# Performance work log

Measured on AMD Instinct MI355X. Metric: run time of the kernel, lower is better.

## Reference

```python
import jax, jax.numpy as jnp
import numpy as np

N_NODES = 100000
N_EDGES = 1600000
NFEAT = 128
NHID = 128
NCLASS = 16


def _sage_conv(x, src, dst, w_self, w_neigh, b):
    # mean aggregation over in-neighbors: for each dst, mean of x[src]
    msgs = x[src]                                   # [E, F] gather
    agg = jax.ops.segment_sum(msgs, dst, num_segments=x.shape[0])  # [N, F]
    deg = jax.ops.segment_sum(jnp.ones((src.shape[0],), x.dtype), dst,
                              num_segments=x.shape[0])             # [N]
    h_neigh = agg / jnp.maximum(deg, 1.0)[:, None]
    return x @ w_self + h_neigh @ w_neigh + b


def setup_inputs() -> dict:
    key = jax.random.key(0)
    ks = jax.random.split(key, 9)
    x = jax.random.normal(ks[0], (N_NODES, NFEAT), dtype=jnp.float32)
    src = jax.random.randint(ks[1], (N_EDGES,), 0, N_NODES, dtype=jnp.int32)
    dst = jax.random.randint(ks[2], (N_EDGES,), 0, N_NODES, dtype=jnp.int32)
    s1 = 1.0 / np.sqrt(NFEAT)
    s2 = 1.0 / np.sqrt(NHID)
    w_self1 = jax.random.uniform(ks[3], (NFEAT, NHID), jnp.float32, -s1, s1)
    w_neigh1 = jax.random.uniform(ks[4], (NFEAT, NHID), jnp.float32, -s1, s1)
    b1 = jnp.zeros((NHID,), jnp.float32)
    w_self2 = jax.random.uniform(ks[5], (NHID, NCLASS), jnp.float32, -s2, s2)
    w_neigh2 = jax.random.uniform(ks[6], (NHID, NCLASS), jnp.float32, -s2, s2)
    b2 = jnp.zeros((NCLASS,), jnp.float32)
    return {"x": x, "src": src, "dst": dst,
            "w_self1": w_self1, "w_neigh1": w_neigh1, "b1": b1,
            "w_self2": w_self2, "w_neigh2": w_neigh2, "b2": b2}


def reference(x, src, dst, w_self1, w_neigh1, b1, w_self2, w_neigh2, b2):
    h = jax.nn.relu(_sage_conv(x, src, dst, w_self1, w_neigh1, b1))
    # dropout is identity in eval mode (training=False)
    out = _sage_conv(h, src, dst, w_self2, w_neigh2, b2)
    return jax.nn.log_softmax(out, axis=1)
```

## Files before the change

kernel.cpp:

```cpp
#include <hip/hip_runtime.h>
#include <math.h>

#define NN 100000
#define NE 1600000
#define BSZ 64
#define NBUCK ((NN + BSZ - 1) / BSZ)
#define NBLK 256
#define CHUNK ((NE + NBLK - 1) / NBLK)
#define NH (NBUCK * NBLK)
#define NSB ((NH + 1023) / 1024)

typedef unsigned int uint;
typedef unsigned short ushort_t;
typedef float f32x2 __attribute__((ext_vector_type(2)));
typedef float f32x4 __attribute__((ext_vector_type(4)));
typedef short s16x8 __attribute__((ext_vector_type(8)));

union U4S8 { uint4 u; s16x8 s; };

__device__ inline uint bf16_1(float f) {
  uint u = __float_as_uint(f);
  return (u + 0x7FFFu + ((u >> 16) & 1u)) >> 16;
}
__device__ inline uint bf16_2(float lo, float hi) {
  return bf16_1(lo) | (bf16_1(hi) << 16);
}

__device__ inline f32x4 mfma_bf16(uint4 a, uint4 b, f32x4 c) {
  U4S8 ua, ub; ua.u = a; ub.u = b;
  return __builtin_amdgcn_mfma_f32_16x16x32_bf16(ua.s, ub.s, c, 0, 0, 0);
}

__global__ __launch_bounds__(256) void tobf16_kernel(
    const float* __restrict__ x, uint* __restrict__ xh,
    uint* __restrict__ xq) {
  int i = blockIdx.x * 256 + threadIdx.x;
  if (i >= NN * 16) return;
  const float4* p = (const float4*)x + (size_t)i * 2;
  float4 a = p[0], b = p[1];
  uint4 o;
  o.x = bf16_2(a.x, a.y);
  o.y = bf16_2(a.z, a.w);
  o.z = bf16_2(b.x, b.y);
  o.w = bf16_2(b.z, b.w);
  ((uint4*)xh)[i] = o;
  int q0 = __builtin_amdgcn_cvt_pk_fp8_f32(a.x, a.y, 0, false);
  q0 = __builtin_amdgcn_cvt_pk_fp8_f32(a.z, a.w, q0, true);
  int q1 = __builtin_amdgcn_cvt_pk_fp8_f32(b.x, b.y, 0, false);
  q1 = __builtin_amdgcn_cvt_pk_fp8_f32(b.z, b.w, q1, true);
  uint2 oq; oq.x = (uint)q0; oq.y = (uint)q1;
  int r = i >> 4;
  int u = (i & 15) * 2;
  *(uint2*)(xq + (size_t)r * 32 + u) = oq;
}

__global__ __launch_bounds__(256) void prep_w_kernel(
    const float* __restrict__ ws1, const float* __restrict__ wn1,
    const float* __restrict__ ws2, const float* __restrict__ wn2,
    uint* __restrict__ w1t, uint* __restrict__ w2t) {
  int idx = blockIdx.x * 256 + threadIdx.x;
  if (idx < 128 * 128) {
    int col = idx >> 7, ku = idx & 127;
    int k = ku * 2;
    const float* w = (k < 128) ? ws1 : wn1;
    int kk = (k < 128) ? k : (k - 128);
    w1t[idx] = bf16_2(w[(size_t)kk * 128 + col], w[(size_t)(kk + 1) * 128 + col]);
  } else if (idx < 128 * 128 + 32 * 64) {
    int j = idx - 128 * 128;
    int col = j >> 6, ku = j & 63;
    int k = ku * 2;
    const float* w = (col < 16) ? ws2 : wn2;
    int c = col & 15;
    w2t[j] = bf16_2(w[(size_t)k * 16 + c], w[(size_t)(k + 1) * 16 + c]);
  }
}

__global__ __launch_bounds__(1024) void histA_kernel(
    const int* __restrict__ dst, int* __restrict__ hist2) {
  __shared__ int lh[NBUCK];
  int tid = threadIdx.x;
  int b = blockIdx.x;
  for (int i = tid; i < NBUCK; i += 1024) lh[i] = 0;
  __syncthreads();
  int e0 = b * CHUNK, e1 = min(e0 + CHUNK, NE);
  for (int e = e0 + tid; e < e1; e += 1024) {
    atomicAdd(&lh[dst[e] >> 6], 1);
  }
  __syncthreads();
  for (int i = tid; i < NBUCK; i += 1024)
    hist2[(size_t)b * NBUCK + i] = lh[i];
}

__global__ __launch_bounds__(1024) void transpose_kernel(
    const int* __restrict__ hist2, int* __restrict__ hist) {
  __shared__ int t[32][33];
  int tx = threadIdx.x & 31, ty = threadIdx.x >> 5;
  int i = blockIdx.x * 32 + tx;
  int b = blockIdx.y * 32 + ty;
  if (i < NBUCK) t[ty][tx] = hist2[(size_t)b * NBUCK + i];
  __syncthreads();
  int i2 = blockIdx.x * 32 + ty;
  int b2 = blockIdx.y * 32 + tx;
  if (i2 < NBUCK) hist[(size_t)i2 * NBLK + b2] = t[tx][ty];
}

__global__ __launch_bounds__(1024) void scan_sums_kernel(
    const int* __restrict__ hist, int* __restrict__ sums) {
  __shared__ int sdata[1024];
  int i = blockIdx.x * 1024 + threadIdx.x;
  sdata[threadIdx.x] = (i < NH) ? hist[i] : 0;
  __syncthreads();
#pragma unroll
  for (int s = 512; s > 0; s >>= 1) {
    if (threadIdx.x < s) sdata[threadIdx.x] += sdata[threadIdx.x + s];
    __syncthreads();
  }
  if (threadIdx.x == 0) sums[blockIdx.x] = sdata[0];
}

__global__ __launch_bounds__(512) void scan_tops_kernel(int* __restrict__ sums) {
  __shared__ int buf[2][512];
  int tid = threadIdx.x;
  int v = (tid < NSB) ? sums[tid] : 0;
  buf[0][tid] = v;
  __syncthreads();
  int pp = 0;
#pragma unroll
  for (int d = 1; d < 512; d <<= 1) {
    buf[pp ^ 1][tid] = buf[pp][tid] + ((tid >= d) ? buf[pp][tid - d] : 0);
    pp ^= 1;
    __syncthreads();
  }
  if (tid < NSB) sums[tid] = buf[pp][tid] - v;
}

__global__ __launch_bounds__(1024) void scan_apply_kernel(
    int* __restrict__ hist, const int* __restrict__ sums) {
  __shared__ int buf[2][1024];
  int tid = threadIdx.x;
  int i = blockIdx.x * 1024 + tid;
  int v = (i < NH) ? hist[i] : 0;
  buf[0][tid] = v;
  __syncthreads();
  int pp = 0;
#pragma unroll
  for (int d = 1; d < 1024; d <<= 1) {
    buf[pp ^ 1][tid] = buf[pp][tid] + ((tid >= d) ? buf[pp][tid - d] : 0);
    pp ^= 1;
    __syncthreads();
  }
  if (i < NH) hist[i] = sums[blockIdx.x] + buf[pp][tid] - v;
}

__global__ __launch_bounds__(1024) void scatter3_kernel(
    const int* __restrict__ src, const int* __restrict__ dst,
    const int* __restrict__ scanned, unsigned int* __restrict__ ebuf) {
  __shared__ int cur[NBUCK];
  int tid = threadIdx.x;
  int b = blockIdx.x;
  for (int i = tid; i < NBUCK; i += 1024) cur[i] = scanned[i * NBLK + b];
  __syncthreads();
  int e0 = b * CHUNK, e1 = min(e0 + CHUNK, NE);
  for (int e = e0 + tid; e < e1; e += 1024) {
    int d = dst[e];
    int p = atomicAdd(&cur[d >> 6], 1);
    ebuf[p] = ((unsigned int)(d & 63) << 17) | (unsigned int)src[e];
  }
}

__global__ __launch_bounds__(256) void bucket_sort_kernel(
    const unsigned int* __restrict__ ebuf, const int* __restrict__ scanned,
    int* __restrict__ deg, int* __restrict__ off, int* __restrict__ perm) {
  __shared__ int cnt[BSZ];
  __shared__ int loc_off[BSZ];
  int tid = threadIdx.x;
  int b = blockIdx.x;
  int e0 = scanned[b * NBLK];
  int e1 = (b + 1 < NBUCK) ? scanned[(b + 1) * NBLK] : NE;

  if (tid < BSZ) cnt[tid] = 0;
  __syncthreads();
  for (int e = e0 + tid; e < e1; e += 256)
    atomicAdd(&cnt[ebuf[e] >> 17], 1);
  __syncthreads();

  if (tid < BSZ) {
    int v = cnt[tid];
    int incl = v;
#pragma unroll
    for (int d = 1; d < 64; d <<= 1) {
      int t = __shfl_up(incl, d);
      if (tid >= d) incl += t;
    }
    int excl = incl - v;
    loc_off[tid] = e0 + excl;
    int node = b * BSZ + tid;
    if (node < NN) { off[node] = e0 + excl; deg[node] = v; }
    cnt[tid] = 0;
  }
  __syncthreads();

  for (int e = e0 + tid; e < e1; e += 256) {
    unsigned int pk = ebuf[e];
    int dl = pk >> 17;
    int p = loc_off[dl] + atomicAdd(&cnt[dl], 1);
    perm[p] = (int)(pk & 0x1FFFF);
  }
}

__global__ __launch_bounds__(256) void mean1_kernel(
    const uint* __restrict__ xq, const int* __restrict__ off,
    const int* __restrict__ deg, const int* __restrict__ perm,
    uint* __restrict__ m1h) {
  int node = blockIdx.x * 4 + (threadIdx.x >> 6);
  int lane = threadIdx.x & 63;
  if (node >= NN) return;
  int o = off[node], dg = deg[node];
  int slot = lane >> 5;
  int q = lane & 31;
  f32x2 a0 = {0.f, 0.f}, a1 = {0.f, 0.f};
  int j = 0;
  for (; j + 8 <= dg; j += 8) {
    int sA = perm[o + j + slot];
    int sB = perm[o + j + 2 + slot];
    int sC = perm[o + j + 4 + slot];
    int sD = perm[o + j + 6 + slot];
    uint vA = xq[(size_t)sA * 32 + q];
    uint vB = xq[(size_t)sB * 32 + q];
    uint vC = xq[(size_t)sC * 32 + q];
    uint vD = xq[(size_t)sD * 32 + q];
    a0 += __builtin_amdgcn_cvt_pk_f32_fp8(vA, 0);
    a1 += __builtin_amdgcn_cvt_pk_f32_fp8(vA, 1);
    a0 += __builtin_amdgcn_cvt_pk_f32_fp8(vB, 0);
    a1 += __builtin_amdgcn_cvt_pk_f32_fp8(vB, 1);
    a0 += __builtin_amdgcn_cvt_pk_f32_fp8(vC, 0);
    a1 += __builtin_amdgcn_cvt_pk_f32_fp8(vC, 1);
    a0 += __builtin_amdgcn_cvt_pk_f32_fp8(vD, 0);
    a1 += __builtin_amdgcn_cvt_pk_f32_fp8(vD, 1);
  }
  for (; j + 2 <= dg; j += 2) {
    int s = perm[o + j + slot];
    uint v = xq[(size_t)s * 32 + q];
    a0 += __builtin_amdgcn_cvt_pk_f32_fp8(v, 0);
    a1 += __builtin_amdgcn_cvt_pk_f32_fp8(v, 1);
  }
  if (j < dg && slot == 0) {
    int s = perm[o + j];
    uint v = xq[(size_t)s * 32 + q];
    a0 += __builtin_amdgcn_cvt_pk_f32_fp8(v, 0);
    a1 += __builtin_amdgcn_cvt_pk_f32_fp8(v, 1);
  }
  a0.x += __shfl_xor(a0.x, 32);
  a0.y += __shfl_xor(a0.y, 32);
  a1.x += __shfl_xor(a1.x, 32);
  a1.y += __shfl_xor(a1.y, 32);
  if (slot == 0) {
    float rd = 1.0f / fmaxf((float)dg, 1.0f);
    uint2 o2;
    o2.x = bf16_2(a0.x * rd, a0.y * rd);
    o2.y = bf16_2(a1.x * rd, a1.y * rd);
    *(uint2*)(m1h + (size_t)node * 64 + q * 2) = o2;
  }
}

__global__ __launch_bounds__(256) void gemm1_mfma_kernel(
    const uint* __restrict__ xh, const uint* __restrict__ m1h,
    const uint* __restrict__ w1t, const float* __restrict__ b1,
    ushort_t* __restrict__ hout) {
  __shared__ uint lds_w[128 * 128];
  int tid = threadIdx.x;

#pragma unroll
  for (int i = 0; i < 16; i++) {
    int g = tid + i * 256;
    int row = g >> 5, c = g & 31;
    uint4 v = ((const uint4*)w1t)[g];
    int cs = c ^ (row & 7);
    *(uint4*)&lds_w[row * 128 + cs * 4] = v;
  }
  __syncthreads();

  int wv = tid >> 6;
  int lane = tid & 63;
  int lr = lane & 15, lk = lane >> 4;
  int r0 = blockIdx.x * 256 + wv * 64;
  if (r0 >= NN) return;

  f32x4 acc[4][8];
#pragma unroll
  for (int i = 0; i < 4; i++)
#pragma unroll
    for (int j = 0; j < 8; j++) acc[i][j] = (f32x4){0.f, 0.f, 0.f, 0.f};

#pragma unroll
  for (int ks = 0; ks < 8; ks++) {
    const uint* A = (ks < 4) ? xh : m1h;
    int ku = (ks & 3) * 16 + lk * 4;
    uint4 a[4];
#pragma unroll
    for (int rt = 0; rt < 4; rt++) {
      int row = r0 + rt * 16 + lr;
      if (row >= NN) row = NN - 1;
      a[rt] = *(const uint4*)(A + (size_t)row * 64 + ku);
    }
    int cbase = ks * 4 + lk;
#pragma unroll
    for (int ct = 0; ct < 8; ct++) {
      int brow = ct * 16 + lr;
      int cs = cbase ^ (lr & 7);
      uint4 bu = *(const uint4*)&lds_w[brow * 128 + cs * 4];
#pragma unroll
      for (int rt = 0; rt < 4; rt++)
        acc[rt][ct] = mfma_bf16(a[rt], bu, acc[rt][ct]);
    }
  }

  float bias[8];
#pragma unroll
  for (int ct = 0; ct < 8; ct++) bias[ct] = b1[ct * 16 + lr];

#pragma unroll
  for (int rt = 0; rt < 4; rt++) {
#pragma unroll
    for (int r = 0; r < 4; r++) {
      int row = r0 + rt * 16 + lk * 4 + r;
      if (row < NN) {
#pragma unroll
        for (int ct = 0; ct < 8; ct++) {
          int col = ct * 16 + lr;
          float v = fmaxf(acc[rt][ct][r] + bias[ct], 0.0f);
          hout[(size_t)row * 128 + col] = (ushort_t)bf16_1(v);
        }
      }
    }
  }
}

__global__ __launch_bounds__(256) void gemm2_mfma_kernel(
    const uint* __restrict__ h, const uint* __restrict__ w2t,
    float* __restrict__ oself, float* __restrict__ h2) {
  int wid = (blockIdx.x * 256 + threadIdx.x) >> 6;
  int lane = threadIdx.x & 63;
  int r0 = wid * 32;
  if (r0 >= NN) return;
  int lr = lane & 15, lk = lane >> 4;

  f32x4 acc[2][2];
#pragma unroll
  for (int i = 0; i < 2; i++)
#pragma unroll
    for (int j = 0; j < 2; j++) acc[i][j] = (f32x4){0.f, 0.f, 0.f, 0.f};

#pragma unroll
  for (int ks = 0; ks < 4; ks++) {
    int ku = ks * 16;
    uint4 a0 = *(const uint4*)(h + (size_t)(r0 + lr) * 64 + ku + lk * 4);
    uint4 a1 = *(const uint4*)(h + (size_t)(r0 + 16 + lr) * 64 + ku + lk * 4);
#pragma unroll
    for (int ct = 0; ct < 2; ct++) {
      uint4 bu = *(const uint4*)(w2t + (size_t)(ct * 16 + lr) * 64 + ku + lk * 4);
      acc[0][ct] = mfma_bf16(a0, bu, acc[0][ct]);
      acc[1][ct] = mfma_bf16(a1, bu, acc[1][ct]);
    }
  }

#pragma unroll
  for (int rt = 0; rt < 2; rt++) {
#pragma unroll
    for (int r = 0; r < 4; r++) {
      int row = r0 + rt * 16 + lk * 4 + r;
      oself[(size_t)row * 16 + lr] = acc[rt][0][r];
      h2[(size_t)row * 16 + lr]    = acc[rt][1][r];
    }
  }
}

__global__ __launch_bounds__(256) void mean2_kernel(
    const float* __restrict__ h2, const int* __restrict__ off,
    const int* __restrict__ deg, const int* __restrict__ perm,
    const float* __restrict__ oself, const float* __restrict__ b2,
    float* __restrict__ out) {
  int node = blockIdx.x * 4 + (threadIdx.x >> 6);
  int lane = threadIdx.x & 63;
  if (node >= NN) return;
  int o = off[node], dg = deg[node];
  int slot = lane >> 4;
  int q = lane & 15;
  float a = 0.f;
  int j = 0;
  for (; j + 8 <= dg; j += 8) {
    int sA = perm[o + j + slot];
    int sB = perm[o + j + 4 + slot];
    a += h2[(size_t)sA * 16 + q];
    a += h2[(size_t)sB * 16 + q];
  }
  for (; j + 4 <= dg; j += 4) {
    int s = perm[o + j + slot];
    a += h2[(size_t)s * 16 + q];
  }
  if (j < dg && j + slot < dg) {
    int s = perm[o + j + slot];
    a += h2[(size_t)s * 16 + q];
  }
  a += __shfl_xor(a, 16);
  a += __shfl_xor(a, 32);
  float rd = 1.0f / fmaxf((float)dg, 1.0f);
  float l = oself[(size_t)node * 16 + q] + b2[q] + a * rd;
  float m = l;
#pragma unroll
  for (int d = 1; d <= 8; d <<= 1) m = fmaxf(m, __shfl_xor(m, d));
  float ex = __expf(l - m);
  float s = ex;
#pragma unroll
  for (int d = 1; d <= 8; d <<= 1) s += __shfl_xor(s, d);
  if (lane < 16) out[(size_t)node * 16 + q] = l - m - logf(s);
}

extern "C" void kernel_launch(void* const* d_in, const int* in_sizes, int n_in,
                              void* d_out, int out_size, void* d_ws, size_t ws_size,
                              hipStream_t stream) {
  const float* x   = (const float*)d_in[0];
  const int*   src = (const int*)d_in[1];
  const int*   dst = (const int*)d_in[2];
  const float* ws1 = (const float*)d_in[3];
  const float* wn1 = (const float*)d_in[4];
  const float* b1  = (const float*)d_in[5];
  const float* ws2 = (const float*)d_in[6];
  const float* wn2 = (const float*)d_in[7];
  const float* b2  = (const float*)d_in[8];
  float* out = (float*)d_out;

  char* p = (char*)d_ws;
  int* deg   = (int*)p;  p += (size_t)NN * 4;
  int* off   = (int*)p;  p += (size_t)NN * 4;
  int* hist  = (int*)p;  p += (size_t)NH * 4;
  int* hist2 = (int*)p;  p += (size_t)NH * 4;
  int* sums  = (int*)p;  p += (size_t)((NSB + 31) & ~31) * 4;
  unsigned int* ebuf = (unsigned int*)p; p += (size_t)NE * 4;
  int* perm = (int*)p;  p += (size_t)NE * 4;
  uint* xh   = (uint*)p; p += (size_t)NN * 64 * 4;
  uint* m1h  = (uint*)p; p += (size_t)NN * 64 * 4;
  uint* hbuf = (uint*)p; p += (size_t)NN * 64 * 4;
  uint* xq   = hbuf;
  uint* w1t  = (uint*)p; p += (size_t)128 * 128 * 4;
  uint* w2t  = (uint*)p; p += (size_t)32 * 64 * 4;
  float* h2    = (float*)p; p += (size_t)NN * 16 * 4;
  float* osf   = (float*)p; p += (size_t)NN * 16 * 4;

  tobf16_kernel<<<(NN * 16 + 255) / 256, 256, 0, stream>>>(x, xh, xq);
  prep_w_kernel<<<(128 * 128 + 32 * 64 + 255) / 256, 256, 0, stream>>>(
      ws1, wn1, ws2, wn2, w1t, w2t);

  histA_kernel<<<NBLK, 1024, 0, stream>>>(dst, hist2);
  transpose_kernel<<<dim3((NBUCK + 31) / 32, NBLK / 32), 1024, 0, stream>>>(
      hist2, hist);
  scan_sums_kernel<<<NSB, 1024, 0, stream>>>(hist, sums);
  scan_tops_kernel<<<1, 512, 0, stream>>>(sums);
  scan_apply_kernel<<<NSB, 1024, 0, stream>>>(hist, sums);
  scatter3_kernel<<<NBLK, 1024, 0, stream>>>(src, dst, hist, ebuf);
  bucket_sort_kernel<<<NBUCK, 256, 0, stream>>>(ebuf, hist, deg, off, perm);

  mean1_kernel<<<(NN + 3) / 4, 256, 0, stream>>>(xq, off, deg, perm, m1h);

  gemm1_mfma_kernel<<<(NN + 255) / 256, 256, 0, stream>>>(
      xh, m1h, w1t, b1, (ushort_t*)hbuf);
  gemm2_mfma_kernel<<<(NN + 127) / 128, 256, 0, stream>>>(hbuf, w2t, osf, h2);

  mean2_kernel<<<(NN + 3) / 4, 256, 0, stream>>>(h2, off, deg, perm, osf, b2, out);
}
```

Measured before the change: 184.9 us.

## Fuse layer-1 and layer-2 GEMMs, keeping hidden activations in LDS

The second-layer GEMM is merged into the first-layer GEMM kernel. The ReLU'd bf16 hidden tile is written to the reused LDS weight buffer with an XOR swizzle and read back directly as MFMA A-operands. This removes the global write and re-read of the 100k x 128 bf16 hidden matrix and one kernel launch. In exchange it adds a block barrier, and the early return for out-of-range waves is dropped so every wave reaches that barrier.

```diff
diff --git a/kernel.cpp b/kernel.cpp
--- a/kernel.cpp
+++ b/kernel.cpp
@@ -263,10 +263,11 @@
   }
 }
 
-__global__ __launch_bounds__(256) void gemm1_mfma_kernel(
+__global__ __launch_bounds__(256) void gemm12_kernel(
     const uint* __restrict__ xh, const uint* __restrict__ m1h,
-    const uint* __restrict__ w1t, const float* __restrict__ b1,
-    ushort_t* __restrict__ hout) {
+    const uint* __restrict__ w1t, const uint* __restrict__ w2t,
+    const float* __restrict__ b1, float* __restrict__ oself,
+    float* __restrict__ h2) {
   __shared__ uint lds_w[128 * 128];
   int tid = threadIdx.x;
 
@@ -284,7 +285,6 @@
   int lane = tid & 63;
   int lr = lane & 15, lk = lane >> 4;
   int r0 = blockIdx.x * 256 + wv * 64;
-  if (r0 >= NN) return;
 
   f32x4 acc[4][8];
 #pragma unroll
@@ -319,58 +319,60 @@
 #pragma unroll
   for (int ct = 0; ct < 8; ct++) bias[ct] = b1[ct * 16 + lr];
 
+  __syncthreads();
+
+  ushort_t* lds_h = (ushort_t*)lds_w;
+#pragma unroll
+  for (int rt = 0; rt < 4; rt++) {
+#pragma unroll
+    for (int r = 0; r < 4; r++) {
+      int rel = wv * 64 + rt * 16 + lk * 4 + r;
+#pragma unroll
+      for (int ct = 0; ct < 8; ct++) {
+        int col = ct * 16 + lr;
+        float v = fmaxf(acc[rt][ct][r] + bias[ct], 0.0f);
+        int chunk = col >> 3;
+        int cs = chunk ^ ((rel & 7) << 1);
+        lds_h[rel * 128 + (cs << 3) + (col & 7)] = (ushort_t)bf16_1(v);
+      }
+    }
+  }
+
+  f32x4 acc2[4][2];
+#pragma unroll
+  for (int i = 0; i < 4; i++)
+#pragma unroll
+    for (int j = 0; j < 2; j++) acc2[i][j] = (f32x4){0.f, 0.f, 0.f, 0.f};
+
+#pragma unroll
+  for (int ks = 0; ks < 4; ks++) {
+    uint4 a[4];
+#pragma unroll
+    for (int rt = 0; rt < 4; rt++) {
+      int rel = wv * 64 + rt * 16 + lr;
+      int chunk = ks * 4 + lk;
+      int cs = chunk ^ ((rel & 7) << 1);
+      a[rt] = *(const uint4*)&lds_h[rel * 128 + (cs << 3)];
+    }
+#pragma unroll
+    for (int ct = 0; ct < 2; ct++) {
+      uint4 bu = *(const uint4*)(w2t + (size_t)(ct * 16 + lr) * 64 + ks * 16 + lk * 4);
+      acc2[0][ct] = mfma_bf16(a[0], bu, acc2[0][ct]);
+      acc2[1][ct] = mfma_bf16(a[1], bu, acc2[1][ct]);
+      acc2[2][ct] = mfma_bf16(a[2], bu, acc2[2][ct]);
+      acc2[3][ct] = mfma_bf16(a[3], bu, acc2[3][ct]);
+    }
+  }
+
 #pragma unroll
   for (int rt = 0; rt < 4; rt++) {
 #pragma unroll
     for (int r = 0; r < 4; r++) {
       int row = r0 + rt * 16 + lk * 4 + r;
       if (row < NN) {
-#pragma unroll
-        for (int ct = 0; ct < 8; ct++) {
-          int col = ct * 16 + lr;
-          float v = fmaxf(acc[rt][ct][r] + bias[ct], 0.0f);
-          hout[(size_t)row * 128 + col] = (ushort_t)bf16_1(v);
-        }
+        oself[(size_t)row * 16 + lr] = acc2[rt][0][r];
+        h2[(size_t)row * 16 + lr]    = acc2[rt][1][r];
       }
-    }
-  }
-}
-
-__global__ __launch_bounds__(256) void gemm2_mfma_kernel(
-    const uint* __restrict__ h, const uint* __restrict__ w2t,
-    float* __restrict__ oself, float* __restrict__ h2) {
-  int wid = (blockIdx.x * 256 + threadIdx.x) >> 6;
-  int lane = threadIdx.x & 63;
-  int r0 = wid * 32;
-  if (r0 >= NN) return;
-  int lr = lane & 15, lk = lane >> 4;
-
-  f32x4 acc[2][2];
-#pragma unroll
-  for (int i = 0; i < 2; i++)
-#pragma unroll
-    for (int j = 0; j < 2; j++) acc[i][j] = (f32x4){0.f, 0.f, 0.f, 0.f};
-
-#pragma unroll
-  for (int ks = 0; ks < 4; ks++) {
-    int ku = ks * 16;
-    uint4 a0 = *(const uint4*)(h + (size_t)(r0 + lr) * 64 + ku + lk * 4);
-    uint4 a1 = *(const uint4*)(h + (size_t)(r0 + 16 + lr) * 64 + ku + lk * 4);
-#pragma unroll
-    for (int ct = 0; ct < 2; ct++) {
-      uint4 bu = *(const uint4*)(w2t + (size_t)(ct * 16 + lr) * 64 + ku + lk * 4);
-      acc[0][ct] = mfma_bf16(a0, bu, acc[0][ct]);
-      acc[1][ct] = mfma_bf16(a1, bu, acc[1][ct]);
-    }
-  }
-
-#pragma unroll
-  for (int rt = 0; rt < 2; rt++) {
-#pragma unroll
-    for (int r = 0; r < 4; r++) {
-      int row = r0 + rt * 16 + lk * 4 + r;
-      oself[(size_t)row * 16 + lr] = acc[rt][0][r];
-      h2[(size_t)row * 16 + lr]    = acc[rt][1][r];
     }
   }
 }
@@ -440,8 +442,7 @@
   int* perm = (int*)p;  p += (size_t)NE * 4;
   uint* xh   = (uint*)p; p += (size_t)NN * 64 * 4;
   uint* m1h  = (uint*)p; p += (size_t)NN * 64 * 4;
-  uint* hbuf = (uint*)p; p += (size_t)NN * 64 * 4;
-  uint* xq   = hbuf;
+  uint* xq   = (uint*)p; p += (size_t)NN * 32 * 4;
   uint* w1t  = (uint*)p; p += (size_t)128 * 128 * 4;
   uint* w2t  = (uint*)p; p += (size_t)32 * 64 * 4;
   float* h2    = (float*)p; p += (size_t)NN * 16 * 4;
@@ -462,9 +463,8 @@
 
   mean1_kernel<<<(NN + 3) / 4, 256, 0, stream>>>(xq, off, deg, perm, m1h);
 
-  gemm1_mfma_kernel<<<(NN + 255) / 256, 256, 0, stream>>>(
-      xh, m1h, w1t, b1, (ushort_t*)hbuf);
-  gemm2_mfma_kernel<<<(NN + 127) / 128, 256, 0, stream>>>(hbuf, w2t, osf, h2);
+  gemm12_kernel<<<(NN + 255) / 256, 256, 0, stream>>>(
+      xh, m1h, w1t, w2t, b1, osf, h2);
 
   mean2_kernel<<<(NN + 3) / 4, 256, 0, stream>>>(h2, off, deg, perm, osf, b2, out);
 }
```

Result: faster. 180.1 us (-2.6%).
